# Kernel tuning notes

Hardware: AMD Instinct MI355X
Metric: run time of the kernel (lower is better)

The kernel has to match this reference:

```python
import jax, jax.numpy as jnp
import numpy as np

N_NODES = 100000
N_EDGES = 1600000
IN_C, HID_C, OUT_C, K = 128, 128, 64, 3


def setup_inputs() -> dict:
    key = jax.random.key(0)
    ks = jax.random.split(key, 8)
    x = jax.random.normal(ks[0], (N_NODES, IN_C), dtype=jnp.float32)
    edge_index = jax.random.randint(ks[1], (2, N_EDGES), 0, N_NODES, dtype=jnp.int64)
    s = 0.05
    W0 = jax.random.normal(ks[2], (K, IN_C, HID_C), dtype=jnp.float32) * s
    b0 = jnp.zeros((HID_C,), dtype=jnp.float32)
    W1 = jax.random.normal(ks[3], (K, HID_C, HID_C), dtype=jnp.float32) * s
    b1 = jnp.zeros((HID_C,), dtype=jnp.float32)
    W2 = jax.random.normal(ks[4], (K, HID_C, OUT_C), dtype=jnp.float32) * s
    b2 = jnp.zeros((OUT_C,), dtype=jnp.float32)
    return {"x": x, "edge_index": edge_index, "W0": W0, "b0": b0,
            "W1": W1, "b1": b1, "W2": W2, "b2": b2}


def reference(x, edge_index, W0, b0, W1, b1, W2, b2):
    # PyG ChebConv with normalization='sym', lambda_max=2.0:
    # L_hat = L - I = -D^{-1/2} A D^{-1/2}  (self-loop weight nets to zero)
    src, dst = edge_index[0], edge_index[1]
    n = x.shape[0]
    deg = jax.ops.segment_sum(jnp.ones(src.shape, x.dtype), src, num_segments=n)
    dinv = jnp.where(deg > 0, jax.lax.rsqrt(deg), 0.0)
    w = -dinv[src] * dinv[dst]  # [E] edge weights of L_hat

    def prop(h):  # y[dst] += w * h[src]  (sparse L_hat @ h)
        return jax.ops.segment_sum(w[:, None] * h[src], dst, num_segments=n)

    def cheb_conv(h, W, b):
        # Tx_0 = h; Tx_1 = L_hat h; Tx_k = 2 L_hat Tx_{k-1} - Tx_{k-2}
        Tx0 = h
        out = Tx0 @ W[0]
        Tx1 = prop(Tx0)
        out = out + Tx1 @ W[1]
        for k in range(2, W.shape[0]):
            Tx2 = 2.0 * prop(Tx1) - Tx0
            out = out + Tx2 @ W[k]
            Tx0, Tx1 = Tx1, Tx2
        return out + b

    h = jax.nn.relu(cheb_conv(x, W0, b0))   # dropout is identity in eval mode
    h = jax.nn.relu(cheb_conv(h, W1, b1))
    return cheb_conv(h, W2, b2)
```

## Files before the change

### kernel.cpp

```cpp
#include <hip/hip_runtime.h>
#include <hip/hip_bf16.h>

#define NN 100000
#define NE 1600000
#define TST 384
#define NB 196
#define BSH 9
#define SCH 4096

typedef __attribute__((ext_vector_type(8))) short short8;
typedef __attribute__((ext_vector_type(4))) float f32x4;

__device__ __forceinline__ unsigned bf16r(float x) {
    unsigned u = __float_as_uint(x);
    return (u + 0x7fffu + ((u >> 16) & 1u)) >> 16;
}
__device__ __forceinline__ unsigned pack_bf16(float a, float b) {
    return bf16r(a) | (bf16r(b) << 16);
}
__device__ __forceinline__ void unpack2(int b, float& lo, float& hi) {
    lo = __uint_as_float(((unsigned)b) << 16);
    hi = __uint_as_float(((unsigned)b) & 0xffff0000u);
}

__global__ __launch_bounds__(256) void hist_kernel(const int* __restrict__ src,
                                                   const int* __restrict__ dst,
                                                   int* __restrict__ binS,
                                                   int* __restrict__ binD, int E) {
    __shared__ int hS[NB], hD[NB];
    for (int i = threadIdx.x; i < NB; i += 256) { hS[i] = 0; hD[i] = 0; }
    __syncthreads();
    for (int e = blockIdx.x * 256 + threadIdx.x; e < E; e += gridDim.x * 256) {
        atomicAdd(&hS[src[e] >> BSH], 1);
        atomicAdd(&hD[dst[e] >> BSH], 1);
    }
    __syncthreads();
    for (int i = threadIdx.x; i < NB; i += 256) {
        if (hS[i]) atomicAdd(&binS[i], hS[i]);
        if (hD[i]) atomicAdd(&binD[i], hD[i]);
    }
}

__global__ void scan_kernel(const int* __restrict__ binS, const int* __restrict__ binD,
                            int* __restrict__ curS, int* __restrict__ offS,
                            int* __restrict__ curD, int* __restrict__ offD,
                            int* __restrict__ rowptr, int E) {
    if (threadIdx.x == 0 && blockIdx.x == 0) {
        int rs = 0, rd = 0;
        for (int i = 0; i < NB; ++i) {
            curS[i] = rs; offS[i] = rs; rs += binS[i];
            curD[i] = rd; offD[i] = rd; rd += binD[i];
        }
        offS[NB] = rs;
        offD[NB] = rd;
        rowptr[NN] = E;
    }
}

__global__ __launch_bounds__(256) void scatter_kernel(const int* __restrict__ src,
                                                      const int* __restrict__ dst,
                                                      int* __restrict__ curS,
                                                      int* __restrict__ curD,
                                                      int* __restrict__ srcB,
                                                      int* __restrict__ packB, int E) {
    __shared__ int cS[NB], cD[NB], bS[NB], bD[NB];
    int base = blockIdx.x * SCH;
    for (int i = threadIdx.x; i < NB; i += 256) { cS[i] = 0; cD[i] = 0; }
    __syncthreads();
    int s[16], d[16], rS[16], rD[16];
#pragma unroll
    for (int k = 0; k < 16; ++k) {
        int idx = base + k * 256 + threadIdx.x;
        if (idx < E) {
            s[k] = src[idx]; d[k] = dst[idx];
            rS[k] = atomicAdd(&cS[s[k] >> BSH], 1);
            rD[k] = atomicAdd(&cD[d[k] >> BSH], 1);
        } else {
            s[k] = -1;
        }
    }
    __syncthreads();
    for (int i = threadIdx.x; i < NB; i += 256) {
        if (cS[i]) bS[i] = atomicAdd(&curS[i], cS[i]);
        if (cD[i]) bD[i] = atomicAdd(&curD[i], cD[i]);
    }
    __syncthreads();
#pragma unroll
    for (int k = 0; k < 16; ++k) {
        if (s[k] >= 0) {
            srcB[bS[s[k] >> BSH] + rS[k]] = s[k];
            packB[bD[d[k] >> BSH] + rD[k]] = s[k] | ((d[k] & 511) << 20);
        }
    }
}

__global__ __launch_bounds__(256) void csr_kernel(const int* __restrict__ offD,
                                                  const int* __restrict__ packB,
                                                  int* __restrict__ rowptr,
                                                  int* __restrict__ csrCol, int n) {
    int b = blockIdx.x;
    int node0 = b << BSH;
    int nNodes = min(512, n - node0);
    if (nNodes <= 0) return;
    int beg = offD[b], end = offD[b + 1];
    __shared__ int h[512];
    __shared__ int roff[512];
    for (int i = threadIdx.x; i < 512; i += 256) h[i] = 0;
    __syncthreads();
    for (int p = beg + threadIdx.x; p < end; p += 256)
        atomicAdd(&h[(packB[p] >> 20) & 511], 1);
    __syncthreads();
    if (threadIdx.x == 0) {
        int r = beg;
        for (int i = 0; i < 512; ++i) { roff[i] = r; r += h[i]; }
    }
    __syncthreads();
    for (int i = threadIdx.x; i < nNodes; i += 256) rowptr[node0 + i] = roff[i];
    for (int i = threadIdx.x; i < 512; i += 256) h[i] = 0;
    __syncthreads();
    for (int p = beg + threadIdx.x; p < end; p += 256) {
        int pk = packB[p];
        int dl = (pk >> 20) & 511;
        int r = atomicAdd(&h[dl], 1);
        csrCol[roff[dl] + r] = pk & 0xFFFFF;
    }
}

__global__ __launch_bounds__(256) void deg_kernel(const int* __restrict__ offS,
                                                  const int* __restrict__ srcB,
                                                  float* __restrict__ dinv, int n) {
    int b = blockIdx.x;
    int node0 = b << BSH;
    int nNodes = min(512, n - node0);
    if (nNodes <= 0) return;
    int beg = offS[b], end = offS[b + 1];
    __shared__ int h[512];
    for (int i = threadIdx.x; i < 512; i += 256) h[i] = 0;
    __syncthreads();
    for (int p = beg + threadIdx.x; p < end; p += 256)
        atomicAdd(&h[srcB[p] & 511], 1);
    __syncthreads();
    for (int i = threadIdx.x; i < nNodes; i += 256) {
        int d = h[i];
        dinv[node0 + i] = d > 0 ? rsqrtf((float)d) : 0.0f;
    }
}

__global__ void copyx_kernel(const float* __restrict__ x, short* __restrict__ T, int n) {
    int i = blockIdx.x * blockDim.x + threadIdx.x;
    int total = n * 32;
    if (i < total) {
        int row = i >> 5, c4 = i & 31;
        float4 v = *(const float4*)(x + (size_t)row * 128 + c4 * 4);
        uint2 o;
        o.x = pack_bf16(v.x, v.y);
        o.y = pack_bf16(v.z, v.w);
        *(uint2*)(T + (size_t)row * TST + c4 * 4) = o;
    }
}

__global__ void convw_kernel(const float* __restrict__ W0, const float* __restrict__ W1,
                             const float* __restrict__ W2, short* __restrict__ Bt0,
                             short* __restrict__ Bt1, short* __restrict__ Bt2) {
    int i = blockIdx.x * blockDim.x + threadIdx.x;
    if (i < 384 * 128) {
        int k = i / 128, c = i % 128;
        Bt0[(size_t)c * 384 + k] = (short)bf16r(W0[i]);
    } else if (i < 2 * 384 * 128) {
        int j = i - 384 * 128;
        int k = j / 128, c = j % 128;
        Bt1[(size_t)c * 384 + k] = (short)bf16r(W1[j]);
    } else if (i < 2 * 384 * 128 + 384 * 64) {
        int j = i - 2 * 384 * 128;
        int k = j / 64, c = j % 64;
        Bt2[(size_t)c * 384 + k] = (short)bf16r(W2[j]);
    }
}

template <int MODE>
__global__ __launch_bounds__(256) void prop_kernel(short* __restrict__ T,
                                                   const int* __restrict__ rowptr,
                                                   const int* __restrict__ csrCol,
                                                   const float* __restrict__ dinv, int n) {
    int wid = (blockIdx.x * blockDim.x + threadIdx.x) >> 6;
    int lane = threadIdx.x & 63;
    if (wid >= n) return;
    int beg = rowptr[wid];
    int c = rowptr[wid + 1] - beg;
    c = min(c, 64);
    constexpr int srcOff = (MODE == 0) ? 0 : 128;
    int myc = 0; float mydv = 0.f;
    if (lane < c) {
        myc = csrCol[beg + lane];
        mydv = dinv[myc];
    }
    int sg = lane >> 4;
    int sl = lane & 15;
    float a0 = 0, a1 = 0, a2 = 0, a3 = 0, a4 = 0, a5 = 0, a6 = 0, a7 = 0;
    for (int base = 0; base < c; base += 16) {
        int j0 = base + sg, j1 = j0 + 4, j2 = j0 + 8, j3 = j0 + 12;
        int   s0 = __shfl(myc, j0);  float w0 = __shfl(mydv, j0);
        int   s1 = __shfl(myc, j1);  float w1 = __shfl(mydv, j1);
        int   s2 = __shfl(myc, j2);  float w2 = __shfl(mydv, j2);
        int   s3 = __shfl(myc, j3);  float w3 = __shfl(mydv, j3);
        int4 v0 = *(const int4*)(T + (size_t)s0 * TST + srcOff + sl * 8);
        int4 v1 = *(const int4*)(T + (size_t)s1 * TST + srcOff + sl * 8);
        int4 v2 = *(const int4*)(T + (size_t)s2 * TST + srcOff + sl * 8);
        int4 v3 = *(const int4*)(T + (size_t)s3 * TST + srcOff + sl * 8);
        float lo, hi;
        unpack2(v0.x, lo, hi); a0 = fmaf(w0, lo, a0); a1 = fmaf(w0, hi, a1);
        unpack2(v0.y, lo, hi); a2 = fmaf(w0, lo, a2); a3 = fmaf(w0, hi, a3);
        unpack2(v0.z, lo, hi); a4 = fmaf(w0, lo, a4); a5 = fmaf(w0, hi, a5);
        unpack2(v0.w, lo, hi); a6 = fmaf(w0, lo, a6); a7 = fmaf(w0, hi, a7);
        unpack2(v1.x, lo, hi); a0 = fmaf(w1, lo, a0); a1 = fmaf(w1, hi, a1);
        unpack2(v1.y, lo, hi); a2 = fmaf(w1, lo, a2); a3 = fmaf(w1, hi, a3);
        unpack2(v1.z, lo, hi); a4 = fmaf(w1, lo, a4); a5 = fmaf(w1, hi, a5);
        unpack2(v1.w, lo, hi); a6 = fmaf(w1, lo, a6); a7 = fmaf(w1, hi, a7);
        unpack2(v2.x, lo, hi); a0 = fmaf(w2, lo, a0); a1 = fmaf(w2, hi, a1);
        unpack2(v2.y, lo, hi); a2 = fmaf(w2, lo, a2); a3 = fmaf(w2, hi, a3);
        unpack2(v2.z, lo, hi); a4 = fmaf(w2, lo, a4); a5 = fmaf(w2, hi, a5);
        unpack2(v2.w, lo, hi); a6 = fmaf(w2, lo, a6); a7 = fmaf(w2, hi, a7);
        unpack2(v3.x, lo, hi); a0 = fmaf(w3, lo, a0); a1 = fmaf(w3, hi, a1);
        unpack2(v3.y, lo, hi); a2 = fmaf(w3, lo, a2); a3 = fmaf(w3, hi, a3);
        unpack2(v3.z, lo, hi); a4 = fmaf(w3, lo, a4); a5 = fmaf(w3, hi, a5);
        unpack2(v3.w, lo, hi); a6 = fmaf(w3, lo, a6); a7 = fmaf(w3, hi, a7);
    }
#define RED(x) x += __shfl_xor(x, 16); x += __shfl_xor(x, 32);
    RED(a0) RED(a1) RED(a2) RED(a3) RED(a4) RED(a5) RED(a6) RED(a7)
#undef RED
    float scale = -dinv[wid] * (MODE ? 2.f : 1.f);
    if (lane < 16) {
        short* o = T + (size_t)wid * TST;
        int4 r;
        if (MODE == 0) {
            r.x = pack_bf16(scale * a0, scale * a1);
            r.y = pack_bf16(scale * a2, scale * a3);
            r.z = pack_bf16(scale * a4, scale * a5);
            r.w = pack_bf16(scale * a6, scale * a7);
            *(int4*)(o + 128 + sl * 8) = r;
        } else {
            int4 t0 = *(const int4*)(o + sl * 8);
            float l, h;
            unpack2(t0.x, l, h);
            r.x = pack_bf16(fmaf(scale, a0, -l), fmaf(scale, a1, -h));
            unpack2(t0.y, l, h);
            r.y = pack_bf16(fmaf(scale, a2, -l), fmaf(scale, a3, -h));
            unpack2(t0.z, l, h);
            r.z = pack_bf16(fmaf(scale, a4, -l), fmaf(scale, a5, -h));
            unpack2(t0.w, l, h);
            r.w = pack_bf16(fmaf(scale, a6, -l), fmaf(scale, a7, -h));
            *(int4*)(o + 256 + sl * 8) = r;
        }
    }
}

template <int BN, int RELU, int OUTF>
__global__ __launch_bounds__(256) void mgemm_kernel(const short* __restrict__ A,
                                                    const short* __restrict__ Bt,
                                                    const float* __restrict__ bias,
                                                    void* __restrict__ Cout,
                                                    int out_stride, int n) {
    constexpr int WAVES_M = (BN == 128) ? 2 : 4;
    constexpr int WM = 128 / WAVES_M;
    constexpr int WN = 64;
    constexpr int MF = WM / 16;
    constexpr int NF = WN / 16;
    constexpr int LDP = 40;
    __shared__ short As[128 * LDP];
    __shared__ short Bs[BN * LDP];

    int tid = threadIdx.x;
    int lane = tid & 63;
    int wid = tid >> 6;
    int wy = (BN == 128) ? (wid >> 1) : wid;
    int wx = (BN == 128) ? (wid & 1) : 0;
    int row0 = blockIdx.x * 128;

    f32x4 acc[MF][NF];
#pragma unroll
    for (int i = 0; i < MF; ++i)
#pragma unroll
        for (int j = 0; j < NF; ++j) acc[i][j] = (f32x4){0.f, 0.f, 0.f, 0.f};

    int l15 = lane & 15;
    int kb = (lane >> 4) * 8;

    for (int k0 = 0; k0 < 384; k0 += 32) {
#pragma unroll
        for (int i = 0; i < 2; ++i) {
            int slot = tid + i * 256;
            int r = slot >> 2, seg = slot & 3;
            int gr = row0 + r;
            short8 v = (short8){0, 0, 0, 0, 0, 0, 0, 0};
            if (gr < n) v = *(const short8*)(A + (size_t)gr * TST + k0 + seg * 8);
            *(short8*)&As[r * LDP + seg * 8] = v;
        }
        constexpr int BSLOTS = BN / 64;
#pragma unroll
        for (int i = 0; i < BSLOTS; ++i) {
            int slot = tid + i * 256;
            int r = slot >> 2, seg = slot & 3;
            *(short8*)&Bs[r * LDP + seg * 8] =
                *(const short8*)(Bt + (size_t)r * 384 + k0 + seg * 8);
        }
        __syncthreads();

        short8 af[MF], bfr[NF];
#pragma unroll
        for (int mf = 0; mf < MF; ++mf)
            af[mf] = *(short8*)&As[(wy * WM + mf * 16 + l15) * LDP + kb];
#pragma unroll
        for (int nf = 0; nf < NF; ++nf)
            bfr[nf] = *(short8*)&Bs[(wx * WN + nf * 16 + l15) * LDP + kb];
#pragma unroll
        for (int mf = 0; mf < MF; ++mf)
#pragma unroll
            for (int nf = 0; nf < NF; ++nf)
                acc[mf][nf] = __builtin_amdgcn_mfma_f32_16x16x32_bf16(
                    af[mf], bfr[nf], acc[mf][nf], 0, 0, 0);
        __syncthreads();
    }

#pragma unroll
    for (int mf = 0; mf < MF; ++mf) {
#pragma unroll
        for (int nf = 0; nf < NF; ++nf) {
            int colc = wx * WN + nf * 16 + l15;
            float bb = bias[colc];
#pragma unroll
            for (int r = 0; r < 4; ++r) {
                int row = row0 + wy * WM + mf * 16 + (lane >> 4) * 4 + r;
                if (row >= n) continue;
                float v = acc[mf][nf][r] + bb;
                if (RELU) v = fmaxf(v, 0.f);
                if (OUTF) {
                    ((float*)Cout)[(size_t)row * out_stride + colc] = v;
                } else {
                    ((short*)Cout)[(size_t)row * TST + colc] = (short)bf16r(v);
                }
            }
        }
    }
}

extern "C" void kernel_launch(void* const* d_in, const int* in_sizes, int n_in,
                              void* d_out, int out_size, void* d_ws, size_t ws_size,
                              hipStream_t stream) {
    const float* x  = (const float*)d_in[0];
    const int*   ei = (const int*)d_in[1];
    const float* W0 = (const float*)d_in[2];
    const float* b0 = (const float*)d_in[3];
    const float* W1 = (const float*)d_in[4];
    const float* b1 = (const float*)d_in[5];
    const float* W2 = (const float*)d_in[6];
    const float* b2 = (const float*)d_in[7];
    float* out = (float*)d_out;

    const int n = NN, E = NE;
    const int* src = ei;
    const int* dst = ei + E;

    char* ws = (char*)d_ws;
    auto alloc = [&](size_t bytes) -> void* {
        void* p = (void*)ws;
        ws += (bytes + 255) & ~(size_t)255;
        return p;
    };
    int*   binS   = (int*)alloc(NB * 4);
    int*   binD   = (int*)alloc(NB * 4);
    int*   curS   = (int*)alloc((NB + 1) * 4);
    int*   offS   = (int*)alloc((NB + 1) * 4);
    int*   curD   = (int*)alloc((NB + 1) * 4);
    int*   offD   = (int*)alloc((NB + 1) * 4);
    int*   srcB   = (int*)alloc((size_t)E * 4);
    int*   packB  = (int*)alloc((size_t)E * 4);
    int*   rowptr = (int*)alloc((size_t)(n + 1) * 4);
    int*   csrCol = (int*)alloc((size_t)E * 4);
    float* dinv   = (float*)alloc((size_t)n * 4);
    short* T      = (short*)alloc((size_t)n * TST * 2);
    short* Bt0    = (short*)alloc((size_t)128 * 384 * 2);
    short* Bt1    = (short*)alloc((size_t)128 * 384 * 2);
    short* Bt2    = (short*)alloc((size_t)64 * 384 * 2);

    hipMemsetAsync(binS, 0, NB * 4, stream);
    hipMemsetAsync(binD, 0, NB * 4, stream);

    const int TPB = 256;

    hist_kernel<<<256, TPB, 0, stream>>>(src, dst, binS, binD, E);
    scan_kernel<<<1, 64, 0, stream>>>(binS, binD, curS, offS, curD, offD, rowptr, E);
    int sChunks = (E + SCH - 1) / SCH;
    scatter_kernel<<<sChunks, TPB, 0, stream>>>(src, dst, curS, curD, srcB, packB, E);
    csr_kernel<<<NB, TPB, 0, stream>>>(offD, packB, rowptr, csrCol, n);
    deg_kernel<<<NB, TPB, 0, stream>>>(offS, srcB, dinv, n);

    convw_kernel<<<(2 * 384 * 128 + 384 * 64 + 255) / 256, 256, 0, stream>>>(
        W0, W1, W2, Bt0, Bt1, Bt2);
    copyx_kernel<<<(n * 32 + TPB - 1) / TPB, TPB, 0, stream>>>(x, T, n);

    int pBlocks = (n + 3) / 4;
    int gBlocks = (n + 127) / 128;

    prop_kernel<0><<<pBlocks, 256, 0, stream>>>(T, rowptr, csrCol, dinv, n);
    prop_kernel<1><<<pBlocks, 256, 0, stream>>>(T, rowptr, csrCol, dinv, n);
    mgemm_kernel<128, 1, 0><<<gBlocks, 256, 0, stream>>>(T, Bt0, b0, T, 0, n);
    prop_kernel<0><<<pBlocks, 256, 0, stream>>>(T, rowptr, csrCol, dinv, n);
    prop_kernel<1><<<pBlocks, 256, 0, stream>>>(T, rowptr, csrCol, dinv, n);
    mgemm_kernel<128, 1, 0><<<gBlocks, 256, 0, stream>>>(T, Bt1, b1, T, 0, n);
    prop_kernel<0><<<pBlocks, 256, 0, stream>>>(T, rowptr, csrCol, dinv, n);
    prop_kernel<1><<<pBlocks, 256, 0, stream>>>(T, rowptr, csrCol, dinv, n);
    mgemm_kernel<64, 0, 1><<<gBlocks, 256, 0, stream>>>(T, Bt2, b2, out, 64, n);
}
```

Baseline: 580.9 us.

## Reorder Chebyshev conv to GEMM-first Horner form with fused propagation epilogues

Each ChebConv is rewritten as h·[W0−W2, W1, 2W2] followed by two nested sparse propagations, P1 + L̂·(2P2) and then P0 + L̂·(...). One 128×384 GEMM per layer now runs before the propagations. In the last layer the propagations work on 64 channels instead of 128, and the 384-wide concatenated T buffer is gone. The fp32→bf16 conversion of x moves into the GEMM load, which drops the copyx kernel. Bias, ReLU and the final fp32 store move into the prop epilogue. The neighbour cap of 64 is replaced with a chunked loop over all neighbours. The cost is extra bf16 intermediate buffers, plus rounding on the weight combinations and on an additional intermediate, which could shift accuracy slightly.

```diff
diff --git a/kernel.cpp b/kernel.cpp
--- a/kernel.cpp
+++ b/kernel.cpp
@@ -3,7 +3,6 @@
 
 #define NN 100000
 #define NE 1600000
-#define TST 384
 #define NB 196
 #define BSH 9
 #define SCH 4096
@@ -146,199 +145,219 @@
     }
 }
 
-__global__ void copyx_kernel(const float* __restrict__ x, short* __restrict__ T, int n) {
-    int i = blockIdx.x * blockDim.x + threadIdx.x;
-    int total = n * 32;
-    if (i < total) {
-        int row = i >> 5, c4 = i & 31;
-        float4 v = *(const float4*)(x + (size_t)row * 128 + c4 * 4);
-        uint2 o;
-        o.x = pack_bf16(v.x, v.y);
-        o.y = pack_bf16(v.z, v.w);
-        *(uint2*)(T + (size_t)row * TST + c4 * 4) = o;
-    }
-}
-
 __global__ void convw_kernel(const float* __restrict__ W0, const float* __restrict__ W1,
                              const float* __restrict__ W2, short* __restrict__ Bt0,
                              short* __restrict__ Bt1, short* __restrict__ Bt2) {
     int i = blockIdx.x * blockDim.x + threadIdx.x;
-    if (i < 384 * 128) {
-        int k = i / 128, c = i % 128;
-        Bt0[(size_t)c * 384 + k] = (short)bf16r(W0[i]);
-    } else if (i < 2 * 384 * 128) {
-        int j = i - 384 * 128;
-        int k = j / 128, c = j % 128;
-        Bt1[(size_t)c * 384 + k] = (short)bf16r(W1[j]);
-    } else if (i < 2 * 384 * 128 + 384 * 64) {
-        int j = i - 2 * 384 * 128;
-        int k = j / 64, c = j % 64;
-        Bt2[(size_t)c * 384 + k] = (short)bf16r(W2[j]);
-    }
-}
-
-template <int MODE>
-__global__ __launch_bounds__(256) void prop_kernel(short* __restrict__ T,
+    if (i < 49152) {
+        int j = i >> 7, k = i & 127;
+        int t = j >> 7, o = j & 127;
+        float v = (t == 0) ? W0[k * 128 + o] - W0[2 * 16384 + k * 128 + o]
+                : (t == 1) ? W0[16384 + k * 128 + o]
+                           : 2.f * W0[2 * 16384 + k * 128 + o];
+        Bt0[j * 128 + k] = (short)bf16r(v);
+    } else if (i < 98304) {
+        int m = i - 49152;
+        int j = m >> 7, k = m & 127;
+        int t = j >> 7, o = j & 127;
+        float v = (t == 0) ? W1[k * 128 + o] - W1[2 * 16384 + k * 128 + o]
+                : (t == 1) ? W1[16384 + k * 128 + o]
+                           : 2.f * W1[2 * 16384 + k * 128 + o];
+        Bt1[j * 128 + k] = (short)bf16r(v);
+    } else if (i < 122880) {
+        int m = i - 98304;
+        int j = m >> 7, k = m & 127;
+        int t = j >> 6, o = j & 63;
+        float v = (t == 0) ? W2[k * 64 + o] - W2[2 * 8192 + k * 64 + o]
+                : (t == 1) ? W2[8192 + k * 64 + o]
+                           : 2.f * W2[2 * 8192 + k * 64 + o];
+        Bt2[j * 128 + k] = (short)bf16r(v);
+    }
+}
+
+template <int C, int AF32>
+__global__ __launch_bounds__(512) void gemm_kernel(const void* Asrc,
+                                                   const short* __restrict__ Bt,
+                                                   const float* __restrict__ bias,
+                                                   short* out0, short* out1, short* out2,
+                                                   int n) {
+    constexpr int BNT = 3 * C;
+    constexpr int WC = BNT / 96;
+    constexpr int WR = 8 / WC;
+    constexpr int WM = 128 / WR;
+    constexpr int MF = WM / 16;
+    constexpr int NF = 6;
+    constexpr int LDP = 40;
+    __shared__ short As[128 * LDP];
+    __shared__ short Bs[BNT * LDP];
+
+    int tid = threadIdx.x;
+    int lane = tid & 63;
+    int wid = tid >> 6;
+    int wy = wid / WC;
+    int wx = wid % WC;
+    int row0 = blockIdx.x * 128;
+    int l15 = lane & 15;
+    int kb = (lane >> 4) * 8;
+
+    f32x4 acc[MF][NF];
+#pragma unroll
+    for (int i = 0; i < MF; ++i)
+#pragma unroll
+        for (int j = 0; j < NF; ++j) acc[i][j] = (f32x4){0.f, 0.f, 0.f, 0.f};
+
+    for (int k0 = 0; k0 < 128; k0 += 32) {
+        {
+            int r = tid >> 2, seg = tid & 3;
+            int gr = row0 + r;
+            short8 v = (short8){0, 0, 0, 0, 0, 0, 0, 0};
+            if (gr < n) {
+                if (AF32) {
+                    const float* xp = (const float*)Asrc + (size_t)gr * 128 + k0 + seg * 8;
+                    float4 f0 = *(const float4*)xp;
+                    float4 f1 = *(const float4*)(xp + 4);
+                    v[0] = (short)bf16r(f0.x); v[1] = (short)bf16r(f0.y);
+                    v[2] = (short)bf16r(f0.z); v[3] = (short)bf16r(f0.w);
+                    v[4] = (short)bf16r(f1.x); v[5] = (short)bf16r(f1.y);
+                    v[6] = (short)bf16r(f1.z); v[7] = (short)bf16r(f1.w);
+                } else {
+                    v = *(const short8*)((const short*)Asrc + (size_t)gr * 128 + k0 + seg * 8);
+                }
+            }
+            *(short8*)&As[r * LDP + seg * 8] = v;
+        }
+        constexpr int BSLOT = BNT * 4;
+#pragma unroll
+        for (int i = 0; i < (BSLOT + 511) / 512; ++i) {
+            int slot = tid + i * 512;
+            if (BSLOT % 512 == 0 || slot < BSLOT) {
+                int j = slot >> 2, seg = slot & 3;
+                *(short8*)&Bs[j * LDP + seg * 8] =
+                    *(const short8*)(Bt + (size_t)j * 128 + k0 + seg * 8);
+            }
+        }
+        __syncthreads();
+
+        short8 af[MF], bfr[NF];
+#pragma unroll
+        for (int mf = 0; mf < MF; ++mf)
+            af[mf] = *(short8*)&As[(wy * WM + mf * 16 + l15) * LDP + kb];
+#pragma unroll
+        for (int nf = 0; nf < NF; ++nf)
+            bfr[nf] = *(short8*)&Bs[(wx * 96 + nf * 16 + l15) * LDP + kb];
+#pragma unroll
+        for (int mf = 0; mf < MF; ++mf)
+#pragma unroll
+            for (int nf = 0; nf < NF; ++nf)
+                acc[mf][nf] = __builtin_amdgcn_mfma_f32_16x16x32_bf16(
+                    af[mf], bfr[nf], acc[mf][nf], 0, 0, 0);
+        __syncthreads();
+    }
+
+#pragma unroll
+    for (int nf = 0; nf < NF; ++nf) {
+        int colc = wx * 96 + nf * 16 + l15;
+        int t = colc / C;
+        int off = colc % C;
+        short* P = (t == 0) ? out0 : (t == 1) ? out1 : out2;
+        float bb = (t == 0) ? bias[off] : 0.f;
+#pragma unroll
+        for (int mf = 0; mf < MF; ++mf) {
+#pragma unroll
+            for (int r = 0; r < 4; ++r) {
+                int row = row0 + wy * WM + mf * 16 + (lane >> 4) * 4 + r;
+                if (row >= n) continue;
+                P[(size_t)row * C + off] = (short)bf16r(acc[mf][nf][r] + bb);
+            }
+        }
+    }
+}
+
+template <int C, int RELU, int OUTF>
+__global__ __launch_bounds__(256) void prop_kernel(const short* __restrict__ G,
+                                                   const short* __restrict__ Add,
+                                                   void* __restrict__ O,
                                                    const int* __restrict__ rowptr,
                                                    const int* __restrict__ csrCol,
                                                    const float* __restrict__ dinv, int n) {
+    constexpr int LPE = C / 8;
+    constexpr int EPG = 64 / LPE;
+    constexpr int STEP = 4 * EPG;
     int wid = (blockIdx.x * blockDim.x + threadIdx.x) >> 6;
     int lane = threadIdx.x & 63;
     if (wid >= n) return;
     int beg = rowptr[wid];
     int c = rowptr[wid + 1] - beg;
-    c = min(c, 64);
-    constexpr int srcOff = (MODE == 0) ? 0 : 128;
-    int myc = 0; float mydv = 0.f;
-    if (lane < c) {
-        myc = csrCol[beg + lane];
-        mydv = dinv[myc];
-    }
-    int sg = lane >> 4;
-    int sl = lane & 15;
+    int sg = lane / LPE;
+    int sl = lane & (LPE - 1);
     float a0 = 0, a1 = 0, a2 = 0, a3 = 0, a4 = 0, a5 = 0, a6 = 0, a7 = 0;
-    for (int base = 0; base < c; base += 16) {
-        int j0 = base + sg, j1 = j0 + 4, j2 = j0 + 8, j3 = j0 + 12;
-        int   s0 = __shfl(myc, j0);  float w0 = __shfl(mydv, j0);
-        int   s1 = __shfl(myc, j1);  float w1 = __shfl(mydv, j1);
-        int   s2 = __shfl(myc, j2);  float w2 = __shfl(mydv, j2);
-        int   s3 = __shfl(myc, j3);  float w3 = __shfl(mydv, j3);
-        int4 v0 = *(const int4*)(T + (size_t)s0 * TST + srcOff + sl * 8);
-        int4 v1 = *(const int4*)(T + (size_t)s1 * TST + srcOff + sl * 8);
-        int4 v2 = *(const int4*)(T + (size_t)s2 * TST + srcOff + sl * 8);
-        int4 v3 = *(const int4*)(T + (size_t)s3 * TST + srcOff + sl * 8);
-        float lo, hi;
-        unpack2(v0.x, lo, hi); a0 = fmaf(w0, lo, a0); a1 = fmaf(w0, hi, a1);
-        unpack2(v0.y, lo, hi); a2 = fmaf(w0, lo, a2); a3 = fmaf(w0, hi, a3);
-        unpack2(v0.z, lo, hi); a4 = fmaf(w0, lo, a4); a5 = fmaf(w0, hi, a5);
-        unpack2(v0.w, lo, hi); a6 = fmaf(w0, lo, a6); a7 = fmaf(w0, hi, a7);
-        unpack2(v1.x, lo, hi); a0 = fmaf(w1, lo, a0); a1 = fmaf(w1, hi, a1);
-        unpack2(v1.y, lo, hi); a2 = fmaf(w1, lo, a2); a3 = fmaf(w1, hi, a3);
-        unpack2(v1.z, lo, hi); a4 = fmaf(w1, lo, a4); a5 = fmaf(w1, hi, a5);
-        unpack2(v1.w, lo, hi); a6 = fmaf(w1, lo, a6); a7 = fmaf(w1, hi, a7);
-        unpack2(v2.x, lo, hi); a0 = fmaf(w2, lo, a0); a1 = fmaf(w2, hi, a1);
-        unpack2(v2.y, lo, hi); a2 = fmaf(w2, lo, a2); a3 = fmaf(w2, hi, a3);
-        unpack2(v2.z, lo, hi); a4 = fmaf(w2, lo, a4); a5 = fmaf(w2, hi, a5);
-        unpack2(v2.w, lo, hi); a6 = fmaf(w2, lo, a6); a7 = fmaf(w2, hi, a7);
-        unpack2(v3.x, lo, hi); a0 = fmaf(w3, lo, a0); a1 = fmaf(w3, hi, a1);
-        unpack2(v3.y, lo, hi); a2 = fmaf(w3, lo, a2); a3 = fmaf(w3, hi, a3);
-        unpack2(v3.z, lo, hi); a4 = fmaf(w3, lo, a4); a5 = fmaf(w3, hi, a5);
-        unpack2(v3.w, lo, hi); a6 = fmaf(w3, lo, a6); a7 = fmaf(w3, hi, a7);
-    }
-#define RED(x) x += __shfl_xor(x, 16); x += __shfl_xor(x, 32);
-    RED(a0) RED(a1) RED(a2) RED(a3) RED(a4) RED(a5) RED(a6) RED(a7)
-#undef RED
-    float scale = -dinv[wid] * (MODE ? 2.f : 1.f);
-    if (lane < 16) {
-        short* o = T + (size_t)wid * TST;
-        int4 r;
-        if (MODE == 0) {
-            r.x = pack_bf16(scale * a0, scale * a1);
-            r.y = pack_bf16(scale * a2, scale * a3);
-            r.z = pack_bf16(scale * a4, scale * a5);
-            r.w = pack_bf16(scale * a6, scale * a7);
-            *(int4*)(o + 128 + sl * 8) = r;
+    for (int b0 = 0; b0 < c; b0 += 64) {
+        int cb = min(64, c - b0);
+        int myc = 0; float mydv = 0.f;
+        if (lane < cb) {
+            myc = csrCol[beg + b0 + lane];
+            mydv = dinv[myc];
+        }
+        for (int base = 0; base < cb; base += STEP) {
+            int j0 = base + sg, j1 = j0 + EPG, j2 = j0 + 2 * EPG, j3 = j0 + 3 * EPG;
+            int   s0 = __shfl(myc, j0);  float w0 = __shfl(mydv, j0);
+            int   s1 = __shfl(myc, j1);  float w1 = __shfl(mydv, j1);
+            int   s2 = __shfl(myc, j2);  float w2 = __shfl(mydv, j2);
+            int   s3 = __shfl(myc, j3);  float w3 = __shfl(mydv, j3);
+            int4 v0 = *(const int4*)(G + (size_t)s0 * C + sl * 8);
+            int4 v1 = *(const int4*)(G + (size_t)s1 * C + sl * 8);
+            int4 v2 = *(const int4*)(G + (size_t)s2 * C + sl * 8);
+            int4 v3 = *(const int4*)(G + (size_t)s3 * C + sl * 8);
+            float lo, hi;
+            unpack2(v0.x, lo, hi); a0 = fmaf(w0, lo, a0); a1 = fmaf(w0, hi, a1);
+            unpack2(v0.y, lo, hi); a2 = fmaf(w0, lo, a2); a3 = fmaf(w0, hi, a3);
+            unpack2(v0.z, lo, hi); a4 = fmaf(w0, lo, a4); a5 = fmaf(w0, hi, a5);
+            unpack2(v0.w, lo, hi); a6 = fmaf(w0, lo, a6); a7 = fmaf(w0, hi, a7);
+            unpack2(v1.x, lo, hi); a0 = fmaf(w1, lo, a0); a1 = fmaf(w1, hi, a1);
+            unpack2(v1.y, lo, hi); a2 = fmaf(w1, lo, a2); a3 = fmaf(w1, hi, a3);
+            unpack2(v1.z, lo, hi); a4 = fmaf(w1, lo, a4); a5 = fmaf(w1, hi, a5);
+            unpack2(v1.w, lo, hi); a6 = fmaf(w1, lo, a6); a7 = fmaf(w1, hi, a7);
+            unpack2(v2.x, lo, hi); a0 = fmaf(w2, lo, a0); a1 = fmaf(w2, hi, a1);
+            unpack2(v2.y, lo, hi); a2 = fmaf(w2, lo, a2); a3 = fmaf(w2, hi, a3);
+            unpack2(v2.z, lo, hi); a4 = fmaf(w2, lo, a4); a5 = fmaf(w2, hi, a5);
+            unpack2(v2.w, lo, hi); a6 = fmaf(w2, lo, a6); a7 = fmaf(w2, hi, a7);
+            unpack2(v3.x, lo, hi); a0 = fmaf(w3, lo, a0); a1 = fmaf(w3, hi, a1);
+            unpack2(v3.y, lo, hi); a2 = fmaf(w3, lo, a2); a3 = fmaf(w3, hi, a3);
+            unpack2(v3.z, lo, hi); a4 = fmaf(w3, lo, a4); a5 = fmaf(w3, hi, a5);
+            unpack2(v3.w, lo, hi); a6 = fmaf(w3, lo, a6); a7 = fmaf(w3, hi, a7);
+        }
+    }
+#pragma unroll
+    for (int off = LPE; off < 64; off <<= 1) {
+        a0 += __shfl_xor(a0, off); a1 += __shfl_xor(a1, off);
+        a2 += __shfl_xor(a2, off); a3 += __shfl_xor(a3, off);
+        a4 += __shfl_xor(a4, off); a5 += __shfl_xor(a5, off);
+        a6 += __shfl_xor(a6, off); a7 += __shfl_xor(a7, off);
+    }
+    if (lane < LPE) {
+        float scale = -dinv[wid];
+        int4 ad = *(const int4*)(Add + (size_t)wid * C + sl * 8);
+        float r0, r1, r2, r3, r4, r5, r6, r7, lo, hi;
+        unpack2(ad.x, lo, hi); r0 = fmaf(scale, a0, lo); r1 = fmaf(scale, a1, hi);
+        unpack2(ad.y, lo, hi); r2 = fmaf(scale, a2, lo); r3 = fmaf(scale, a3, hi);
+        unpack2(ad.z, lo, hi); r4 = fmaf(scale, a4, lo); r5 = fmaf(scale, a5, hi);
+        unpack2(ad.w, lo, hi); r6 = fmaf(scale, a6, lo); r7 = fmaf(scale, a7, hi);
+        if (RELU) {
+            r0 = fmaxf(r0, 0.f); r1 = fmaxf(r1, 0.f); r2 = fmaxf(r2, 0.f);
+            r3 = fmaxf(r3, 0.f); r4 = fmaxf(r4, 0.f); r5 = fmaxf(r5, 0.f);
+            r6 = fmaxf(r6, 0.f); r7 = fmaxf(r7, 0.f);
+        }
+        if (OUTF) {
+            float* op = (float*)O + (size_t)wid * C + sl * 8;
+            *(float4*)op = make_float4(r0, r1, r2, r3);
+            *(float4*)(op + 4) = make_float4(r4, r5, r6, r7);
         } else {
-            int4 t0 = *(const int4*)(o + sl * 8);
-            float l, h;
-            unpack2(t0.x, l, h);
-            r.x = pack_bf16(fmaf(scale, a0, -l), fmaf(scale, a1, -h));
-            unpack2(t0.y, l, h);
-            r.y = pack_bf16(fmaf(scale, a2, -l), fmaf(scale, a3, -h));
-            unpack2(t0.z, l, h);
-            r.z = pack_bf16(fmaf(scale, a4, -l), fmaf(scale, a5, -h));
-            unpack2(t0.w, l, h);
-            r.w = pack_bf16(fmaf(scale, a6, -l), fmaf(scale, a7, -h));
-            *(int4*)(o + 256 + sl * 8) = r;
-        }
-    }
-}
-
-template <int BN, int RELU, int OUTF>
-__global__ __launch_bounds__(256) void mgemm_kernel(const short* __restrict__ A,
-                                                    const short* __restrict__ Bt,
-                                                    const float* __restrict__ bias,
-                                                    void* __restrict__ Cout,
-                                                    int out_stride, int n) {
-    constexpr int WAVES_M = (BN == 128) ? 2 : 4;
-    constexpr int WM = 128 / WAVES_M;
-    constexpr int WN = 64;
-    constexpr int MF = WM / 16;
-    constexpr int NF = WN / 16;
-    constexpr int LDP = 40;
-    __shared__ short As[128 * LDP];
-    __shared__ short Bs[BN * LDP];
-
-    int tid = threadIdx.x;
-    int lane = tid & 63;
-    int wid = tid >> 6;
-    int wy = (BN == 128) ? (wid >> 1) : wid;
-    int wx = (BN == 128) ? (wid & 1) : 0;
-    int row0 = blockIdx.x * 128;
-
-    f32x4 acc[MF][NF];
-#pragma unroll
-    for (int i = 0; i < MF; ++i)
-#pragma unroll
-        for (int j = 0; j < NF; ++j) acc[i][j] = (f32x4){0.f, 0.f, 0.f, 0.f};
-
-    int l15 = lane & 15;
-    int kb = (lane >> 4) * 8;
-
-    for (int k0 = 0; k0 < 384; k0 += 32) {
-#pragma unroll
-        for (int i = 0; i < 2; ++i) {
-            int slot = tid + i * 256;
-            int r = slot >> 2, seg = slot & 3;
-            int gr = row0 + r;
-            short8 v = (short8){0, 0, 0, 0, 0, 0, 0, 0};
-            if (gr < n) v = *(const short8*)(A + (size_t)gr * TST + k0 + seg * 8);
-            *(short8*)&As[r * LDP + seg * 8] = v;
-        }
-        constexpr int BSLOTS = BN / 64;
-#pragma unroll
-        for (int i = 0; i < BSLOTS; ++i) {
-            int slot = tid + i * 256;
-            int r = slot >> 2, seg = slot & 3;
-            *(short8*)&Bs[r * LDP + seg * 8] =
-                *(const short8*)(Bt + (size_t)r * 384 + k0 + seg * 8);
-        }
-        __syncthreads();
-
-        short8 af[MF], bfr[NF];
-#pragma unroll
-        for (int mf = 0; mf < MF; ++mf)
-            af[mf] = *(short8*)&As[(wy * WM + mf * 16 + l15) * LDP + kb];
-#pragma unroll
-        for (int nf = 0; nf < NF; ++nf)
-            bfr[nf] = *(short8*)&Bs[(wx * WN + nf * 16 + l15) * LDP + kb];
-#pragma unroll
-        for (int mf = 0; mf < MF; ++mf)
-#pragma unroll
-            for (int nf = 0; nf < NF; ++nf)
-                acc[mf][nf] = __builtin_amdgcn_mfma_f32_16x16x32_bf16(
-                    af[mf], bfr[nf], acc[mf][nf], 0, 0, 0);
-        __syncthreads();
-    }
-
-#pragma unroll
-    for (int mf = 0; mf < MF; ++mf) {
-#pragma unroll
-        for (int nf = 0; nf < NF; ++nf) {
-            int colc = wx * WN + nf * 16 + l15;
-            float bb = bias[colc];
-#pragma unroll
-            for (int r = 0; r < 4; ++r) {
-                int row = row0 + wy * WM + mf * 16 + (lane >> 4) * 4 + r;
-                if (row >= n) continue;
-                float v = acc[mf][nf][r] + bb;
-                if (RELU) v = fmaxf(v, 0.f);
-                if (OUTF) {
-                    ((float*)Cout)[(size_t)row * out_stride + colc] = v;
-                } else {
-                    ((short*)Cout)[(size_t)row * TST + colc] = (short)bf16r(v);
-                }
-            }
+            int4 w;
+            w.x = pack_bf16(r0, r1);
+            w.y = pack_bf16(r2, r3);
+            w.z = pack_bf16(r4, r5);
+            w.w = pack_bf16(r6, r7);
+            *(int4*)((short*)O + (size_t)wid * C + sl * 8) = w;
         }
     }
 }
@@ -377,10 +396,13 @@
     int*   rowptr = (int*)alloc((size_t)(n + 1) * 4);
     int*   csrCol = (int*)alloc((size_t)E * 4);
     float* dinv   = (float*)alloc((size_t)n * 4);
-    short* T      = (short*)alloc((size_t)n * TST * 2);
-    short* Bt0    = (short*)alloc((size_t)128 * 384 * 2);
-    short* Bt1    = (short*)alloc((size_t)128 * 384 * 2);
-    short* Bt2    = (short*)alloc((size_t)64 * 384 * 2);
+    short* buf0   = (short*)alloc((size_t)n * 128 * 2);
+    short* buf1   = (short*)alloc((size_t)n * 128 * 2);
+    short* buf2   = (short*)alloc((size_t)n * 128 * 2);
+    short* buf3   = (short*)alloc((size_t)n * 128 * 2);
+    short* Bt0    = (short*)alloc((size_t)384 * 128 * 2);
+    short* Bt1    = (short*)alloc((size_t)384 * 128 * 2);
+    short* Bt2    = (short*)alloc((size_t)192 * 128 * 2);
 
     hipMemsetAsync(binS, 0, NB * 4, stream);
     hipMemsetAsync(binD, 0, NB * 4, stream);
@@ -394,20 +416,20 @@
     csr_kernel<<<NB, TPB, 0, stream>>>(offD, packB, rowptr, csrCol, n);
     deg_kernel<<<NB, TPB, 0, stream>>>(offS, srcB, dinv, n);
 
-    convw_kernel<<<(2 * 384 * 128 + 384 * 64 + 255) / 256, 256, 0, stream>>>(
-        W0, W1, W2, Bt0, Bt1, Bt2);
-    copyx_kernel<<<(n * 32 + TPB - 1) / TPB, TPB, 0, stream>>>(x, T, n);
+    convw_kernel<<<(122880 + 255) / 256, 256, 0, stream>>>(W0, W1, W2, Bt0, Bt1, Bt2);
 
     int pBlocks = (n + 3) / 4;
     int gBlocks = (n + 127) / 128;
 
-    prop_kernel<0><<<pBlocks, 256, 0, stream>>>(T, rowptr, csrCol, dinv, n);
-    prop_kernel<1><<<pBlocks, 256, 0, stream>>>(T, rowptr, csrCol, dinv, n);
-    mgemm_kernel<128, 1, 0><<<gBlocks, 256, 0, stream>>>(T, Bt0, b0, T, 0, n);
-    prop_kernel<0><<<pBlocks, 256, 0, stream>>>(T, rowptr, csrCol, dinv, n);
-    prop_kernel<1><<<pBlocks, 256, 0, stream>>>(T, rowptr, csrCol, dinv, n);
-    mgemm_kernel<128, 1, 0><<<gBlocks, 256, 0, stream>>>(T, Bt1, b1, T, 0, n);
-    prop_kernel<0><<<pBlocks, 256, 0, stream>>>(T, rowptr, csrCol, dinv, n);
-    prop_kernel<1><<<pBlocks, 256, 0, stream>>>(T, rowptr, csrCol, dinv, n);
-    mgemm_kernel<64, 0, 1><<<gBlocks, 256, 0, stream>>>(T, Bt2, b2, out, 64, n);
-}
+    gemm_kernel<128, 1><<<gBlocks, 512, 0, stream>>>(x, Bt0, b0, buf0, buf1, buf2, n);
+    prop_kernel<128, 0, 0><<<pBlocks, 256, 0, stream>>>(buf2, buf1, buf3, rowptr, csrCol, dinv, n);
+    prop_kernel<128, 1, 0><<<pBlocks, 256, 0, stream>>>(buf3, buf0, buf1, rowptr, csrCol, dinv, n);
+    gemm_kernel<128, 0><<<gBlocks, 512, 0, stream>>>(buf1, Bt1, b1, buf0, buf1, buf2, n);
+    prop_kernel<128, 0, 0><<<pBlocks, 256, 0, stream>>>(buf2, buf1, buf3, rowptr, csrCol, dinv, n);
+    prop_kernel<128, 1, 0><<<pBlocks, 256, 0, stream>>>(buf3, buf0, buf1, rowptr, csrCol, dinv, n);
+    gemm_kernel<64, 0><<<gBlocks, 512, 0, stream>>>(buf1, Bt2, b2, buf0, buf3, buf2, n);
+    prop_kernel<64, 0, 0><<<pBlocks, 256, 0, stream>>>(buf2, buf3, buf0 + (size_t)n * 64,
+                                                       rowptr, csrCol, dinv, n);
+    prop_kernel<64, 0, 1><<<pBlocks, 256, 0, stream>>>(buf0 + (size_t)n * 64, buf0, out,
+                                                       rowptr, csrCol, dinv, n);
+}
```

Measured after the change: 592.3 us. Within noise of the previous version (+2.0%).
